# Optimization experiments

Measured on AMD Instinct MI355X. Metric: run time of the kernel, lower is better.

The kernel has to match this reference:

```python
import jax, jax.numpy as jnp
import numpy as np
from jax import lax

ACTIVE_TOKENS = 256

def setup_inputs() -> dict:
    key = jax.random.key(0)
    k1, k2, k3, k4, k5 = jax.random.split(key, 5)
    B, L, D, A = 8, 4096, 1024, 256
    return {
        "x": jax.random.normal(k1, (B, L, D), dtype=jnp.float32),
        "active": jax.random.normal(k2, (B, A, D), dtype=jnp.float32),
        "cold": jax.random.normal(k3, (B, D), dtype=jnp.float32),
        "w_sal": jax.random.normal(k4, (D,), dtype=jnp.float32) * 0.02,
        "w_read": jax.random.normal(k5, (D, D), dtype=jnp.float32) * 0.02,
    }

def reference(x, active, cold, w_sal, w_read):
    # combined: [B, A+L, D]
    combined = jnp.concatenate([active, x], axis=1)
    B, Lc, D = combined.shape
    keep = min(ACTIVE_TOKENS, Lc)
    # salience head: Linear(D, 1, bias=False) -> [B, Lc]
    salience = jnp.einsum("bld,d->bl", combined, w_sal)
    _, top_idx = lax.top_k(salience, keep)          # [B, keep]
    top_idx = jnp.sort(top_idx, axis=-1)
    # gather kept tokens; torch detaches new_active before use
    kept = jnp.take_along_axis(combined, top_idx[:, :, None], axis=1)  # [B, keep, D]
    new_active = lax.stop_gradient(kept)
    # dropped-token mean (masked_select compaction == total minus kept)
    n_dropped = Lc - keep  # static > 0 here
    dropped_mean = (combined.sum(axis=1) - kept.sum(axis=1)) / n_dropped  # [B, D]
    cold_new = 0.9 * cold + 0.1 * dropped_mean
    # contexts and residual read projection
    active_ctx = new_active.mean(axis=1)            # [B, D]
    ctx = active_ctx + cold_new                      # [B, D]
    x_out = x + jnp.einsum("bd,ed->be", ctx, w_read)[:, None, :]  # Linear: ctx @ W^T
    return x_out, new_active, lax.stop_gradient(cold_new)
```

## Files before the change

kernel.cpp:

```cpp
#include <hip/hip_runtime.h>

#define B 8
#define XROWS 4096
#define AROWS 256
#define LC 4352
#define DD 1024
#define KEEP 256

typedef float vfloat4 __attribute__((ext_vector_type(4)));

__device__ __forceinline__ void nt_store4(const float4& v, float* p) {
    vfloat4 t = {v.x, v.y, v.z, v.w};
    __builtin_nontemporal_store(t, (vfloat4*)p);
}

__device__ __forceinline__ const float* combined_row(const float* __restrict__ x,
                                                     const float* __restrict__ act,
                                                     int b, int l) {
    return (l < AROWS) ? (act + ((size_t)b * AROWS + l) * DD)
                       : (x + ((size_t)b * XROWS + (l - AROWS)) * DD);
}

__global__ __launch_bounds__(256) void k_zero(float* __restrict__ p, int n) {
    int i = blockIdx.x * 256 + threadIdx.x;
    if (i < n) p[i] = 0.0f;
}

__global__ __launch_bounds__(256) void k_sal_sums(
        const float* __restrict__ x, const float* __restrict__ act,
        const float* __restrict__ wsal, float* __restrict__ sal,
        float* __restrict__ sums) {
    const int tid  = threadIdx.x;
    const int wave = tid >> 6;
    const int lane = tid & 63;
    const int b     = blockIdx.x / 136;
    const int chunk = blockIdx.x % 136;
    const int row0  = chunk * 32;
    const int c0 = lane * 4;

    const float4 w0 = *(const float4*)(wsal + 0 * 256 + c0);
    const float4 w1 = *(const float4*)(wsal + 1 * 256 + c0);
    const float4 w2 = *(const float4*)(wsal + 2 * 256 + c0);
    const float4 w3 = *(const float4*)(wsal + 3 * 256 + c0);

    float4 s0 = make_float4(0,0,0,0), s1 = s0, s2 = s0, s3 = s0;

    for (int r = wave; r < 32; r += 4) {
        const int l = row0 + r;
        const float* rp = combined_row(x, act, b, l);
        const float4 a0 = *(const float4*)(rp + 0 * 256 + c0);
        const float4 a1 = *(const float4*)(rp + 1 * 256 + c0);
        const float4 a2 = *(const float4*)(rp + 2 * 256 + c0);
        const float4 a3 = *(const float4*)(rp + 3 * 256 + c0);
        s0.x += a0.x; s0.y += a0.y; s0.z += a0.z; s0.w += a0.w;
        s1.x += a1.x; s1.y += a1.y; s1.z += a1.z; s1.w += a1.w;
        s2.x += a2.x; s2.y += a2.y; s2.z += a2.z; s2.w += a2.w;
        s3.x += a3.x; s3.y += a3.y; s3.z += a3.z; s3.w += a3.w;
        float s = a0.x*w0.x + a0.y*w0.y + a0.z*w0.z + a0.w*w0.w
                + a1.x*w1.x + a1.y*w1.y + a1.z*w1.z + a1.w*w1.w
                + a2.x*w2.x + a2.y*w2.y + a2.z*w2.z + a2.w*w2.w
                + a3.x*w3.x + a3.y*w3.y + a3.z*w3.z + a3.w*w3.w;
        #pragma unroll
        for (int m = 32; m >= 1; m >>= 1) s += __shfl_xor(s, m, 64);
        if (lane == 0) sal[b * LC + l] = s;
    }

    __shared__ float acc[4][DD];
    float* aw = acc[wave];
    *(float4*)(aw + 0 * 256 + c0) = s0;
    *(float4*)(aw + 1 * 256 + c0) = s1;
    *(float4*)(aw + 2 * 256 + c0) = s2;
    *(float4*)(aw + 3 * 256 + c0) = s3;
    __syncthreads();
    const int col = tid * 4;
    float4 t0 = *(const float4*)(acc[0] + col);
    float4 t1 = *(const float4*)(acc[1] + col);
    float4 t2 = *(const float4*)(acc[2] + col);
    float4 t3 = *(const float4*)(acc[3] + col);
    float* sb = sums + b * DD;
    atomicAdd(sb + col + 0, t0.x + t1.x + t2.x + t3.x);
    atomicAdd(sb + col + 1, t0.y + t1.y + t2.y + t3.y);
    atomicAdd(sb + col + 2, t0.z + t1.z + t2.z + t3.z);
    atomicAdd(sb + col + 3, t0.w + t1.w + t2.w + t3.w);
}

__global__ __launch_bounds__(1024) void k_topk(const float* __restrict__ sal,
                                               int* __restrict__ idx,
                                               float* __restrict__ ksum) {
    const int b = blockIdx.x;
    const int tid = threadIdx.x;
    const int lane = tid & 63;
    __shared__ unsigned keys[LC];
    __shared__ int hist[256];
    __shared__ int wtot4[4];
    __shared__ int wtot16[16];
    __shared__ unsigned prefS;
    __shared__ int kremS;

    if (tid < DD) ksum[b * DD + tid] = 0.0f;

    for (int i = tid; i < LC; i += 1024) {
        unsigned u = __float_as_uint(sal[b * LC + i]);
        keys[i] = (u & 0x80000000u) ? ~u : (u | 0x80000000u);
    }
    if (tid == 0) { prefS = 0u; kremS = KEEP; }
    __syncthreads();

    for (int pass = 0; pass < 4; ++pass) {
        const int shift = 24 - 8 * pass;
        if (tid < 256) hist[tid] = 0;
        __syncthreads();
        const unsigned pref = prefS;
        const int krem = kremS;
        for (int i = tid; i < LC; i += 1024) {
            const unsigned k = keys[i];
            if (pass == 0 || (k >> (shift + 8)) == (pref >> (shift + 8)))
                atomicAdd(&hist[(k >> shift) & 255], 1);
        }
        __syncthreads();
        int h = 0, cum = 0;
        if (tid < 256) {
            h = hist[tid];
            cum = h;
            #pragma unroll
            for (int off = 1; off <= 32; off <<= 1) {
                int v = __shfl_down(cum, off, 64);
                if (lane + off < 64) cum += v;
            }
            if (lane == 0) wtot4[tid >> 6] = cum;
        }
        __syncthreads();
        if (tid < 256) {
            for (int w2 = (tid >> 6) + 1; w2 < 4; ++w2) cum += wtot4[w2];
            if (cum >= krem && (cum - h) < krem) {
                prefS = pref | ((unsigned)tid << shift);
                kremS = krem - (cum - h);
            }
        }
        __syncthreads();
    }

    const unsigned T = prefS;
    const int needEQ = kremS;

    const int start = tid * 5;
    const int end = (start + 5 < LC) ? (start + 5) : LC;
    int gt = 0, eq = 0;
    for (int i = start; i < end; ++i) {
        const unsigned k = keys[i];
        gt += (k > T);
        eq += (k == T);
    }
    int packed = (gt << 16) | eq;
    int p = packed;
    #pragma unroll
    for (int off = 1; off <= 32; off <<= 1) {
        int v = __shfl_up(p, off, 64);
        if (lane >= off) p += v;
    }
    if (lane == 63) wtot16[tid >> 6] = p;
    __syncthreads();
    int base = 0;
    for (int w2 = 0; w2 < (tid >> 6); ++w2) base += wtot16[w2];
    const int exc = p - packed + base;
    int gtB = exc >> 16;
    int eqB = exc & 0xFFFF;
    for (int i = start; i < end; ++i) {
        const unsigned k = keys[i];
        if (k > T) {
            idx[b * KEEP + gtB + min(eqB, needEQ)] = i;
            ++gtB;
        } else if (k == T) {
            if (eqB < needEQ) idx[b * KEEP + gtB + eqB] = i;
            ++eqB;
        }
    }
}

__global__ __launch_bounds__(256) void k_gather(const float* __restrict__ x,
        const float* __restrict__ act, const int* __restrict__ idx,
        float* __restrict__ out_active, float* __restrict__ ksum) {
    const int b = blockIdx.x >> 3;
    const int chunk = blockIdx.x & 7;
    const int tid = threadIdx.x;
    const int c4 = tid * 4;
    float4 cs = make_float4(0,0,0,0);
    for (int r = 0; r < 32; ++r) {
        const int k = chunk * 32 + r;
        const int l = idx[b * KEEP + k];
        const float4 v = *(const float4*)(combined_row(x, act, b, l) + c4);
        nt_store4(v, out_active + ((size_t)b * KEEP + k) * DD + c4);
        cs.x += v.x; cs.y += v.y; cs.z += v.z; cs.w += v.w;
    }
    float* kb = ksum + b * DD;
    atomicAdd(kb + c4 + 0, cs.x);
    atomicAdd(kb + c4 + 1, cs.y);
    atomicAdd(kb + c4 + 2, cs.z);
    atomicAdd(kb + c4 + 3, cs.w);
}

__global__ __launch_bounds__(256) void k_read(const float* __restrict__ sums,
        const float* __restrict__ ksum, const float* __restrict__ cold,
        const float* __restrict__ wread, float* __restrict__ rvec,
        float* __restrict__ out_cold) {
    const int blk = blockIdx.x;
    const int tid = threadIdx.x;
    const int wave = tid >> 6;
    const int lane = tid & 63;
    const int c4 = tid * 4;
    __shared__ float ctxs[B][DD];

    #pragma unroll
    for (int bb = 0; bb < B; ++bb) {
        const float4 s  = *(const float4*)(sums + bb * DD + c4);
        const float4 ks = *(const float4*)(ksum + bb * DD + c4);
        const float4 cd = *(const float4*)(cold + bb * DD + c4);
        float4 cn, cx;
        cn.x = 0.9f * cd.x + 0.1f * ((s.x - ks.x) * (1.0f / 4096.0f));
        cn.y = 0.9f * cd.y + 0.1f * ((s.y - ks.y) * (1.0f / 4096.0f));
        cn.z = 0.9f * cd.z + 0.1f * ((s.z - ks.z) * (1.0f / 4096.0f));
        cn.w = 0.9f * cd.w + 0.1f * ((s.w - ks.w) * (1.0f / 4096.0f));
        cx.x = ks.x * (1.0f / 256.0f) + cn.x;
        cx.y = ks.y * (1.0f / 256.0f) + cn.y;
        cx.z = ks.z * (1.0f / 256.0f) + cn.z;
        cx.w = ks.w * (1.0f / 256.0f) + cn.w;
        *(float4*)(&ctxs[bb][c4]) = cx;
        if (blk == 0) *(float4*)(out_cold + bb * DD + c4) = cn;
    }
    __syncthreads();

    const int e = (blk << 2) | wave;
    const int l0 = lane * 4;
    const float* wr = wread + (size_t)e * DD;
    const float4 w0 = *(const float4*)(wr + 0 * 256 + l0);
    const float4 w1 = *(const float4*)(wr + 1 * 256 + l0);
    const float4 w2 = *(const float4*)(wr + 2 * 256 + l0);
    const float4 w3 = *(const float4*)(wr + 3 * 256 + l0);
    #pragma unroll
    for (int bb = 0; bb < B; ++bb) {
        const float4 c0 = *(const float4*)(&ctxs[bb][0 * 256 + l0]);
        const float4 c1 = *(const float4*)(&ctxs[bb][1 * 256 + l0]);
        const float4 c2 = *(const float4*)(&ctxs[bb][2 * 256 + l0]);
        const float4 c3 = *(const float4*)(&ctxs[bb][3 * 256 + l0]);
        float p = w0.x*c0.x + w0.y*c0.y + w0.z*c0.z + w0.w*c0.w
                + w1.x*c1.x + w1.y*c1.y + w1.z*c1.z + w1.w*c1.w
                + w2.x*c2.x + w2.y*c2.y + w2.z*c2.z + w2.w*c2.w
                + w3.x*c3.x + w3.y*c3.y + w3.z*c3.z + w3.w*c3.w;
        #pragma unroll
        for (int m = 32; m >= 1; m >>= 1) p += __shfl_xor(p, m, 64);
        if (lane == 0) rvec[bb * DD + e] = p;
    }
}

__global__ __launch_bounds__(256) void k_xout(const float* __restrict__ x,
        const float* __restrict__ rvec, float* __restrict__ xout) {
    const size_t base = (size_t)blockIdx.x * 1024 + threadIdx.x;
    const float4* x4 = (const float4*)x;
    const float4* r4 = (const float4*)rvec;
    float* of = (float*)xout;

    float4 v0 = x4[base + 0 * 256];
    float4 v1 = x4[base + 1 * 256];
    float4 v2 = x4[base + 2 * 256];
    float4 v3 = x4[base + 3 * 256];
    const int e4 = (int)(base & 255);
    const int bb = (int)(base >> 20);
    const float4 r = r4[(bb << 8) | e4];
    v0.x += r.x; v0.y += r.y; v0.z += r.z; v0.w += r.w;
    v1.x += r.x; v1.y += r.y; v1.z += r.z; v1.w += r.w;
    v2.x += r.x; v2.y += r.y; v2.z += r.z; v2.w += r.w;
    v3.x += r.x; v3.y += r.y; v3.z += r.z; v3.w += r.w;
    nt_store4(v0, of + (base + 0 * 256) * 4);
    nt_store4(v1, of + (base + 1 * 256) * 4);
    nt_store4(v2, of + (base + 2 * 256) * 4);
    nt_store4(v3, of + (base + 3 * 256) * 4);
}

extern "C" void kernel_launch(void* const* d_in, const int* in_sizes, int n_in,
                              void* d_out, int out_size, void* d_ws, size_t ws_size,
                              hipStream_t stream) {
    (void)in_sizes; (void)n_in; (void)out_size; (void)ws_size;
    const float* x     = (const float*)d_in[0];
    const float* act   = (const float*)d_in[1];
    const float* cold  = (const float*)d_in[2];
    const float* wsal  = (const float*)d_in[3];
    const float* wread = (const float*)d_in[4];

    float* out        = (float*)d_out;
    float* xout       = out;
    float* out_active = xout + (size_t)B * XROWS * DD;
    float* out_cold   = out_active + (size_t)B * KEEP * DD;

    float* ws   = (float*)d_ws;
    float* sal  = ws;
    float* sums = sal + B * LC;
    float* ksum = sums + B * DD;
    float* rvec = ksum + B * DD;
    int*   idx  = (int*)(rvec + B * DD);

    k_zero<<<(B * DD + 255) / 256, 256, 0, stream>>>(sums, B * DD);
    k_sal_sums<<<B * 136, 256, 0, stream>>>(x, act, wsal, sal, sums);
    k_topk<<<B, 1024, 0, stream>>>(sal, idx, ksum);
    k_gather<<<B * 8, 256, 0, stream>>>(x, act, idx, out_active, ksum);
    k_read<<<256, 256, 0, stream>>>(sums, ksum, cold, wread, rvec, out_cold);
    k_xout<<<8192, 256, 0, stream>>>(x, rvec, xout);
}
```

Measured before the change: 306.9 us.

## Split read projection algebraically and overlap the sums part with top-k

The context is rewritten as 0.9*cold + sums/40960 + (159/40960)*ksum, so the W_read product over cold and sums runs in extra blocks of the top-k launch, which otherwise uses only 8 blocks. The read kernel then only adds the ksum term. The salience kernel writes order-preserving keys directly, and the gather uses twice as many blocks with half the rows each. This hides part of the matvec behind the serial top-k, at the cost of a second pass over W_read and slightly different float rounding.

```diff
diff --git a/kernel.cpp b/kernel.cpp
--- a/kernel.cpp
+++ b/kernel.cpp
@@ -6,6 +6,8 @@
 #define LC 4352
 #define DD 1024
 #define KEEP 256
+#define BETA  (1.0f / 40960.0f)
+#define ALPHA (159.0f / 40960.0f)
 
 typedef float vfloat4 __attribute__((ext_vector_type(4)));
 
@@ -28,7 +30,7 @@
 
 __global__ __launch_bounds__(256) void k_sal_sums(
         const float* __restrict__ x, const float* __restrict__ act,
-        const float* __restrict__ wsal, float* __restrict__ sal,
+        const float* __restrict__ wsal, unsigned* __restrict__ keysg,
         float* __restrict__ sums) {
     const int tid  = threadIdx.x;
     const int wave = tid >> 6;
@@ -62,7 +64,10 @@
                 + a3.x*w3.x + a3.y*w3.y + a3.z*w3.z + a3.w*w3.w;
         #pragma unroll
         for (int m = 32; m >= 1; m >>= 1) s += __shfl_xor(s, m, 64);
-        if (lane == 0) sal[b * LC + l] = s;
+        if (lane == 0) {
+            const unsigned u = __float_as_uint(s);
+            keysg[b * LC + l] = (u & 0x80000000u) ? ~u : (u | 0x80000000u);
+        }
     }
 
     __shared__ float acc[4][DD];
@@ -84,12 +89,50 @@
     atomicAdd(sb + col + 3, t0.w + t1.w + t2.w + t3.w);
 }
 
-__global__ __launch_bounds__(1024) void k_topk(const float* __restrict__ sal,
+__global__ __launch_bounds__(1024) void k_topk(const unsigned* __restrict__ keysg,
+                                               const float* __restrict__ sums,
+                                               const float* __restrict__ cold,
+                                               const float* __restrict__ wread,
                                                int* __restrict__ idx,
-                                               float* __restrict__ ksum) {
-    const int b = blockIdx.x;
+                                               float* __restrict__ ksum,
+                                               float* __restrict__ rpart) {
+    const int nb = blockIdx.x;
     const int tid = threadIdx.x;
+    const int wave = tid >> 6;
     const int lane = tid & 63;
+
+    if (nb >= 8) {
+        const int gb = nb - 8;
+        const int el = wave >> 2;
+        const int q  = wave & 3;
+        const int e  = (gb << 2) | el;
+        const int c0 = (q << 8) | (lane << 2);
+        __shared__ float gpart[4][4][B];
+        const float4 w4 = *(const float4*)(wread + (size_t)e * DD + c0);
+        #pragma unroll
+        for (int bb = 0; bb < B; ++bb) {
+            const float4 cd = *(const float4*)(cold + bb * DD + c0);
+            const float4 sm = *(const float4*)(sums + bb * DD + c0);
+            float p = w4.x * (0.9f * cd.x + BETA * sm.x)
+                    + w4.y * (0.9f * cd.y + BETA * sm.y)
+                    + w4.z * (0.9f * cd.z + BETA * sm.z)
+                    + w4.w * (0.9f * cd.w + BETA * sm.w);
+            #pragma unroll
+            for (int m = 32; m >= 1; m >>= 1) p += __shfl_xor(p, m, 64);
+            if (lane == 0) gpart[el][q][bb] = p;
+        }
+        __syncthreads();
+        if (tid < 32) {
+            const int el2 = tid >> 3;
+            const int bb  = tid & 7;
+            rpart[bb * DD + ((gb << 2) | el2)] =
+                gpart[el2][0][bb] + gpart[el2][1][bb] +
+                gpart[el2][2][bb] + gpart[el2][3][bb];
+        }
+        return;
+    }
+
+    const int b = nb;
     __shared__ unsigned keys[LC];
     __shared__ int hist[256];
     __shared__ int wtot4[4];
@@ -99,10 +142,7 @@
 
     if (tid < DD) ksum[b * DD + tid] = 0.0f;
 
-    for (int i = tid; i < LC; i += 1024) {
-        unsigned u = __float_as_uint(sal[b * LC + i]);
-        keys[i] = (u & 0x80000000u) ? ~u : (u | 0x80000000u);
-    }
+    for (int i = tid; i < LC; i += 1024) keys[i] = keysg[b * LC + i];
     if (tid == 0) { prefS = 0u; kremS = KEEP; }
     __syncthreads();
 
@@ -180,13 +220,14 @@
 __global__ __launch_bounds__(256) void k_gather(const float* __restrict__ x,
         const float* __restrict__ act, const int* __restrict__ idx,
         float* __restrict__ out_active, float* __restrict__ ksum) {
-    const int b = blockIdx.x >> 3;
-    const int chunk = blockIdx.x & 7;
+    const int b = blockIdx.x >> 4;
+    const int chunk = blockIdx.x & 15;
     const int tid = threadIdx.x;
     const int c4 = tid * 4;
     float4 cs = make_float4(0,0,0,0);
-    for (int r = 0; r < 32; ++r) {
-        const int k = chunk * 32 + r;
+    #pragma unroll 4
+    for (int r = 0; r < 16; ++r) {
+        const int k = chunk * 16 + r;
         const int l = idx[b * KEEP + k];
         const float4 v = *(const float4*)(combined_row(x, act, b, l) + c4);
         nt_store4(v, out_active + ((size_t)b * KEEP + k) * DD + c4);
@@ -199,35 +240,30 @@
     atomicAdd(kb + c4 + 3, cs.w);
 }
 
-__global__ __launch_bounds__(256) void k_read(const float* __restrict__ sums,
-        const float* __restrict__ ksum, const float* __restrict__ cold,
-        const float* __restrict__ wread, float* __restrict__ rvec,
-        float* __restrict__ out_cold) {
+__global__ __launch_bounds__(256) void k_read(const float* __restrict__ ksum,
+        const float* __restrict__ sums, const float* __restrict__ cold,
+        const float* __restrict__ wread, const float* __restrict__ rpart,
+        float* __restrict__ rvec, float* __restrict__ out_cold) {
     const int blk = blockIdx.x;
     const int tid = threadIdx.x;
     const int wave = tid >> 6;
     const int lane = tid & 63;
-    const int c4 = tid * 4;
-    __shared__ float ctxs[B][DD];
-
-    #pragma unroll
-    for (int bb = 0; bb < B; ++bb) {
-        const float4 s  = *(const float4*)(sums + bb * DD + c4);
-        const float4 ks = *(const float4*)(ksum + bb * DD + c4);
-        const float4 cd = *(const float4*)(cold + bb * DD + c4);
-        float4 cn, cx;
-        cn.x = 0.9f * cd.x + 0.1f * ((s.x - ks.x) * (1.0f / 4096.0f));
-        cn.y = 0.9f * cd.y + 0.1f * ((s.y - ks.y) * (1.0f / 4096.0f));
-        cn.z = 0.9f * cd.z + 0.1f * ((s.z - ks.z) * (1.0f / 4096.0f));
-        cn.w = 0.9f * cd.w + 0.1f * ((s.w - ks.w) * (1.0f / 4096.0f));
-        cx.x = ks.x * (1.0f / 256.0f) + cn.x;
-        cx.y = ks.y * (1.0f / 256.0f) + cn.y;
-        cx.z = ks.z * (1.0f / 256.0f) + cn.z;
-        cx.w = ks.w * (1.0f / 256.0f) + cn.w;
-        *(float4*)(&ctxs[bb][c4]) = cx;
-        if (blk == 0) *(float4*)(out_cold + bb * DD + c4) = cn;
-    }
-    __syncthreads();
+
+    if (blk == 0) {
+        const int c4 = tid * 4;
+        #pragma unroll
+        for (int bb = 0; bb < B; ++bb) {
+            const float4 s  = *(const float4*)(sums + bb * DD + c4);
+            const float4 ks = *(const float4*)(ksum + bb * DD + c4);
+            const float4 cd = *(const float4*)(cold + bb * DD + c4);
+            float4 cn;
+            cn.x = 0.9f * cd.x + (s.x - ks.x) * (1.0f / 40960.0f);
+            cn.y = 0.9f * cd.y + (s.y - ks.y) * (1.0f / 40960.0f);
+            cn.z = 0.9f * cd.z + (s.z - ks.z) * (1.0f / 40960.0f);
+            cn.w = 0.9f * cd.w + (s.w - ks.w) * (1.0f / 40960.0f);
+            *(float4*)(out_cold + bb * DD + c4) = cn;
+        }
+    }
 
     const int e = (blk << 2) | wave;
     const int l0 = lane * 4;
@@ -238,17 +274,17 @@
     const float4 w3 = *(const float4*)(wr + 3 * 256 + l0);
     #pragma unroll
     for (int bb = 0; bb < B; ++bb) {
-        const float4 c0 = *(const float4*)(&ctxs[bb][0 * 256 + l0]);
-        const float4 c1 = *(const float4*)(&ctxs[bb][1 * 256 + l0]);
-        const float4 c2 = *(const float4*)(&ctxs[bb][2 * 256 + l0]);
-        const float4 c3 = *(const float4*)(&ctxs[bb][3 * 256 + l0]);
-        float p = w0.x*c0.x + w0.y*c0.y + w0.z*c0.z + w0.w*c0.w
-                + w1.x*c1.x + w1.y*c1.y + w1.z*c1.z + w1.w*c1.w
-                + w2.x*c2.x + w2.y*c2.y + w2.z*c2.z + w2.w*c2.w
-                + w3.x*c3.x + w3.y*c3.y + w3.z*c3.z + w3.w*c3.w;
+        const float4 k0 = *(const float4*)(ksum + bb * DD + 0 * 256 + l0);
+        const float4 k1 = *(const float4*)(ksum + bb * DD + 1 * 256 + l0);
+        const float4 k2 = *(const float4*)(ksum + bb * DD + 2 * 256 + l0);
+        const float4 k3 = *(const float4*)(ksum + bb * DD + 3 * 256 + l0);
+        float p = w0.x*k0.x + w0.y*k0.y + w0.z*k0.z + w0.w*k0.w
+                + w1.x*k1.x + w1.y*k1.y + w1.z*k1.z + w1.w*k1.w
+                + w2.x*k2.x + w2.y*k2.y + w2.z*k2.z + w2.w*k2.w
+                + w3.x*k3.x + w3.y*k3.y + w3.z*k3.z + w3.w*k3.w;
         #pragma unroll
         for (int m = 32; m >= 1; m >>= 1) p += __shfl_xor(p, m, 64);
-        if (lane == 0) rvec[bb * DD + e] = p;
+        if (lane == 0) rvec[bb * DD + e] = rpart[bb * DD + e] + ALPHA * p;
     }
 }
 
@@ -291,17 +327,18 @@
     float* out_active = xout + (size_t)B * XROWS * DD;
     float* out_cold   = out_active + (size_t)B * KEEP * DD;
 
-    float* ws   = (float*)d_ws;
-    float* sal  = ws;
-    float* sums = sal + B * LC;
-    float* ksum = sums + B * DD;
-    float* rvec = ksum + B * DD;
-    int*   idx  = (int*)(rvec + B * DD);
+    float* ws    = (float*)d_ws;
+    unsigned* keysg = (unsigned*)ws;
+    float* sums  = ws + B * LC;
+    float* ksum  = sums + B * DD;
+    float* rvec  = ksum + B * DD;
+    float* rpart = rvec + B * DD;
+    int*   idx   = (int*)(rpart + B * DD);
 
     k_zero<<<(B * DD + 255) / 256, 256, 0, stream>>>(sums, B * DD);
-    k_sal_sums<<<B * 136, 256, 0, stream>>>(x, act, wsal, sal, sums);
-    k_topk<<<B, 1024, 0, stream>>>(sal, idx, ksum);
-    k_gather<<<B * 8, 256, 0, stream>>>(x, act, idx, out_active, ksum);
-    k_read<<<256, 256, 0, stream>>>(sums, ksum, cold, wread, rvec, out_cold);
+    k_sal_sums<<<B * 136, 256, 0, stream>>>(x, act, wsal, keysg, sums);
+    k_topk<<<264, 1024, 0, stream>>>(keysg, sums, cold, wread, idx, ksum, rpart);
+    k_gather<<<B * 16, 256, 0, stream>>>(x, act, idx, out_active, ksum);
+    k_read<<<256, 256, 0, stream>>>(ksum, sums, cold, wread, rpart, rvec, out_cold);
     k_xout<<<8192, 256, 0, stream>>>(x, rvec, xout);
 }
```

Measured after the change: 303.1 us. Within noise of the previous version (-1.2%).
